# Optimization experiments

Hardware: AMD Instinct MI355X
Metric: run time of the kernel (lower is better)

## Reference

```python
import jax, jax.numpy as jnp
import numpy as np
import math

D_MODEL = 1024
D_ATTN = 128
D_MID = 128
L = 4096

def setup_inputs() -> dict:
    key = jax.random.key(0)
    ks = jax.random.split(key, 5)
    scale = 1.0 / math.sqrt(D_MODEL)
    return {
        "x": jax.random.normal(ks[0], (L, D_MODEL), jnp.float32),
        "z": jax.random.normal(ks[1], (L, D_MODEL), jnp.float32),
        "Wq": jax.random.normal(ks[2], (D_MODEL, D_ATTN), jnp.float32) * scale,
        "bq": jnp.zeros((D_ATTN,), jnp.float32),
        "Wk": jax.random.normal(ks[3], (D_MODEL, D_ATTN), jnp.float32) * scale,
        "bk": jnp.zeros((D_ATTN,), jnp.float32),
        "Wv": jax.random.normal(ks[4], (D_MODEL, D_MID), jnp.float32) * scale,
        "bv": jnp.zeros((D_MID,), jnp.float32),
    }

def reference(x, z, Wq, bq, Wk, bk, Wv, bv):
    # q: [L_x, d_attn], k: [L_z, d_attn], v: [L_z, d_mid]
    q = x @ Wq + bq
    k = z @ Wk + bk
    v = z @ Wv + bv
    inv_sqrt_d = 1.0 / math.sqrt(D_ATTN)
    s = (q @ k.T) * inv_sqrt_d            # [L_x, L_z]
    y = jax.nn.softmax(s, axis=-1) @ v    # [L_x, d_mid]
    return y
```

## Files before the change

kernel.cpp:

```cpp
#include <hip/hip_runtime.h>
#include <hip/hip_bf16.h>

typedef __attribute__((ext_vector_type(8))) short short8;
typedef __attribute__((ext_vector_type(4))) float f32x4;
typedef __attribute__((ext_vector_type(8))) _Float16 half8;

#define L_SEQ 4096
#define DM    1024
#define DA    128
#define AZ    16

#define OFF_QB  786432
#define OFF_KF  1835008
#define OFF_VF  2883584
#define OFF_OA  4063232
#define OA_BYTES ((size_t)AZ * L_SEQ * DA * 2)

__device__ __forceinline__ short f2bf(float f) {
    union { float f; unsigned u; } v; v.f = f;
    unsigned u = v.u;
    u += 0x7FFFu + ((u >> 16) & 1u);
    return (short)(u >> 16);
}

__device__ __forceinline__ unsigned cvt_pk_bf16(float lo, float hi) {
    unsigned r;
    asm("v_cvt_pk_bf16_f32 %0, %1, %2" : "=v"(r) : "v"(lo), "v"(hi));
    return r;
}

typedef const __attribute__((address_space(1))) void g_void_t;
typedef __attribute__((address_space(3))) void l_void_t;
__device__ __forceinline__ void g2lds16(const void* g, void* l) {
    __builtin_amdgcn_global_load_lds((g_void_t*)g, (l_void_t*)l, 16, 0, 0);
}

__global__ __launch_bounds__(256) void prep_w_kernel(
    const float* __restrict__ Wq, const float* __restrict__ Wk,
    const float* __restrict__ Wv, short8* __restrict__ WTf)
{
    const int m = blockIdx.y, kidx = blockIdx.x;
    const float* __restrict__ W = (m == 0) ? Wq : (m == 1) ? Wk : Wv;
    __shared__ __align__(16) float Ws[32 * 132];
    const int t = threadIdx.x;
#pragma unroll
    for (int i = 0; i < 4; i++) {
        const int u = i * 256 + t;
        const int kk = u >> 5, n4 = (u & 31) * 4;
        *(f32x4*)&Ws[kk * 132 + n4] = *(const f32x4*)&W[(size_t)(kidx * 32 + kk) * DA + n4];
    }
    __syncthreads();
#pragma unroll
    for (int i = 0; i < 2; i++) {
        const int u = i * 256 + t;
        const int nt = u >> 6, lane = u & 63, l16 = lane & 15, quad = lane >> 4;
        short8 fr;
#pragma unroll
        for (int j = 0; j < 8; j++)
            fr[j] = f2bf(Ws[(quad * 8 + j) * 132 + nt * 16 + l16]);
        WTf[((size_t)(m * 32 + kidx) * 8 + nt) * 64 + lane] = fr;
    }
}

__global__ __launch_bounds__(256, 1) void qkv_kernel(
    const float* __restrict__ x, const float* __restrict__ z,
    const char* __restrict__ WTraw,
    const float* __restrict__ bq, const float* __restrict__ bk,
    const float* __restrict__ bv,
    short* __restrict__ qb, short8* __restrict__ kf, short8* __restrict__ vf)
{
    __shared__ __align__(16) char smem[2][32768];

    const int t = threadIdx.x;
    const int wave = t >> 6, lane = t & 63;
    const int l16 = lane & 15, quad = lane >> 4;
    const int mtile = wave >> 1, nhalf = wave & 1;
    const int isKV = blockIdx.y;
    const int m1 = isKV ? 1 : 0;
    const int row0 = blockIdx.x * 32;
    const int nbytes = isKV ? 32768 : 16384;

    const float* __restrict__ Am = isKV ? z : x;
    const float* ap = Am + (size_t)(row0 + mtile * 16 + l16) * DM + quad * 8;

    f32x4 acc1[4], acc2[4];
#pragma unroll
    for (int i = 0; i < 4; i++) {
        acc1[i] = (f32x4){0.f, 0.f, 0.f, 0.f};
        acc2[i] = (f32x4){0.f, 0.f, 0.f, 0.f};
    }

    auto stage = [&](int it2, int b) {
        const char* base1 = WTraw + (size_t)(m1 * 32 + it2 * 2) * 8192;
        const char* base2 = WTraw + (size_t)(2 * 32 + it2 * 2) * 8192;
#pragma unroll
        for (int i = 0; i < 8; i++) {
            const int off = i * 4096 + wave * 1024;
            if (off < nbytes) {
                const char* src = (off < 16384) ? (base1 + off) : (base2 + (off - 16384));
                g2lds16(src + lane * 16, &smem[b][off]);
            }
        }
    };

    f32x4 cur[4], nxt[4];
#pragma unroll
    for (int j = 0; j < 2; j++) {
        cur[j * 2]     = *(const f32x4*)(ap + j * 32);
        cur[j * 2 + 1] = *(const f32x4*)(ap + j * 32 + 4);
        nxt[j * 2]     = *(const f32x4*)(ap + 64 + j * 32);
        nxt[j * 2 + 1] = *(const f32x4*)(ap + 64 + j * 32 + 4);
    }

    stage(0, 0);
    __syncthreads();

#pragma unroll 1
    for (int it = 0; it < 16; it++) {
        const int b = it & 1;
        if (it + 1 < 16) stage(it + 1, b ^ 1);

        const int ipf = (it + 2 < 16) ? it + 2 : it;
        f32x4 fut[4];
#pragma unroll
        for (int j = 0; j < 2; j++) {
            fut[j * 2]     = *(const f32x4*)(ap + ipf * 64 + j * 32);
            fut[j * 2 + 1] = *(const f32x4*)(ap + ipf * 64 + j * 32 + 4);
        }

#pragma unroll
        for (int ss = 0; ss < 2; ss++) {
            short8 afr;
#pragma unroll
            for (int j = 0; j < 4; j++) {
                afr[j]     = f2bf(cur[ss * 2][j]);
                afr[4 + j] = f2bf(cur[ss * 2 + 1][j]);
            }
#pragma unroll
            for (int ntl = 0; ntl < 4; ntl++) {
                short8 bfr = *(const short8*)&smem[b][ss * 8192 + ((nhalf * 4 + ntl) * 64 + lane) * 16];
                acc1[ntl] = __builtin_amdgcn_mfma_f32_16x16x32_bf16(afr, bfr, acc1[ntl], 0, 0, 0);
            }
            if (isKV) {
#pragma unroll
                for (int ntl = 0; ntl < 4; ntl++) {
                    short8 bfr = *(const short8*)&smem[b][16384 + ss * 8192 + ((nhalf * 4 + ntl) * 64 + lane) * 16];
                    acc2[ntl] = __builtin_amdgcn_mfma_f32_16x16x32_bf16(afr, bfr, acc2[ntl], 0, 0, 0);
                }
            }
        }
        __syncthreads();
#pragma unroll
        for (int j = 0; j < 4; j++) { cur[j] = nxt[j]; nxt[j] = fut[j]; }
    }

    if (!isKV) {
        const float CL2E = 0.1275187669712930f;
#pragma unroll
        for (int ntl = 0; ntl < 4; ntl++) {
            const int col = nhalf * 64 + ntl * 16 + l16;
            const float bb = bq[col];
#pragma unroll
            for (int r = 0; r < 4; r++)
                qb[(size_t)(row0 + mtile * 16 + quad * 4 + r) * DA + col] =
                    f2bf((acc1[ntl][r] + bb) * CL2E);
        }
        return;
    }

    short* kT = (short*)&smem[0][0];
    short* vT = (short*)&smem[0][16384];
#pragma unroll
    for (int ntl = 0; ntl < 4; ntl++) {
        const int col = nhalf * 64 + ntl * 16 + l16;
        const float bbk = bk[col], bbv = bv[col];
#pragma unroll
        for (int r = 0; r < 4; r++) {
            const int rl = mtile * 16 + quad * 4 + r;
            kT[rl * 132 + col] = f2bf(acc1[ntl][r] + bbk);
            vT[rl * 132 + col] = f2bf(acc2[ntl][r] + bbv);
        }
    }
    __syncthreads();

    const int kg = blockIdx.x;
#pragma unroll
    for (int i = 0; i < 2; i++) {
        const int f = i * 256 + t;
        const int ks = f >> 7, nth = (f >> 6) & 1, ln = f & 63;
        const int lf = ln & 15, qf = ln >> 4;
        short8 fr;
#pragma unroll
        for (int j = 0; j < 8; j++)
            fr[j] = kT[(nth * 16 + lf) * 132 + ks * 32 + qf * 8 + j];
        kf[((size_t)(kg * 4 + ks) * 2 + nth) * 64 + ln] = fr;
    }
#pragma unroll
    for (int i = 0; i < 2; i++) {
        const int f = i * 256 + t;
        const int nt = f >> 6, ln = f & 63;
        const int lf = ln & 15, qf = ln >> 4;
        short8 fr;
#pragma unroll
        for (int j = 0; j < 8; j++)
            fr[j] = vT[(qf * 8 + j) * 132 + nt * 16 + lf];
        vf[((size_t)kg * 8 + nt) * 64 + ln] = fr;
    }
}

__global__ __launch_bounds__(256, 2) void attn_kernel(
    const short* __restrict__ qb, const char* __restrict__ kfg,
    const char* __restrict__ vfg, _Float16* __restrict__ OA,
    float* __restrict__ lA)
{
    __shared__ __align__(16) char kv[2][16384];
    __shared__ __align__(16) short Ps[4][2][32 * 40];

    const int t    = threadIdx.x;
    const int wave = t >> 6;
    const int lane = t & 63;
    const int l16  = lane & 15;
    const int quad = lane >> 4;
    const int qr0  = blockIdx.x * 128;
    const int g0   = blockIdx.y * 8;

    auto stage = [&](int g, int b) {
        const char* kb_ = kfg + (size_t)(g0 + g) * 8192;
        const char* vb_ = vfg + (size_t)(g0 + g) * 8192;
#pragma unroll
        for (int i = 0; i < 4; i++) {
            const int off = i * 4096 + wave * 1024;
            const char* src = (off < 8192) ? (kb_ + off) : (vb_ + (off - 8192));
            g2lds16(src + lane * 16, &kv[b][off]);
        }
    };

    stage(0, 0);

    short8 af[2][4];
#pragma unroll
    for (int mt = 0; mt < 2; mt++) {
        const short* qrow = qb + (size_t)(qr0 + wave * 32 + mt * 16 + l16) * DA + quad * 8;
#pragma unroll
        for (int ks = 0; ks < 4; ks++)
            af[mt][ks] = *(const short8*)(qrow + ks * 32);
    }

    short8 bones;
#pragma unroll
    for (int j = 0; j < 8; j++) bones[j] = (l16 == 0) ? (short)0x3F80 : (short)0;

    f32x4 O[2][9];
#pragma unroll
    for (int mt = 0; mt < 2; mt++)
#pragma unroll
        for (int i = 0; i < 9; i++) O[mt][i] = (f32x4){0.f, 0.f, 0.f, 0.f};

    short8 bvC[8];

    __syncthreads();

#pragma unroll 1
    for (int g = 0; g < 8; g++) {
        const int b = g & 1;
        if (g + 1 < 8) stage(g + 1, b ^ 1);

        const char* kb_ = &kv[b][0];
        const char* vb_ = &kv[b][8192];

        f32x4 s0[2][2];
#pragma unroll
        for (int mt = 0; mt < 2; mt++)
#pragma unroll
            for (int nh = 0; nh < 2; nh++) s0[mt][nh] = (f32x4){0.f, 0.f, 0.f, 0.f};
#pragma unroll
        for (int ks = 0; ks < 4; ks++)
#pragma unroll
            for (int nh = 0; nh < 2; nh++) {
                const short8 bfr = *(const short8*)(kb_ + ((ks * 2 + nh) * 64 + lane) * 16);
                s0[0][nh] = __builtin_amdgcn_mfma_f32_16x16x32_bf16(af[0][ks], bfr, s0[0][nh], 0, 0, 0);
                s0[1][nh] = __builtin_amdgcn_mfma_f32_16x16x32_bf16(af[1][ks], bfr, s0[1][nh], 0, 0, 0);
            }

        short8 bvN[8];
#pragma unroll
        for (int nt = 0; nt < 8; nt++)
            bvN[nt] = *(const short8*)(vb_ + (nt * 64 + lane) * 16);

        short8 a2[2];
        if (g > 0) {
            const short* Pp = &Ps[wave][b ^ 1][0];
            a2[0] = *(const short8*)&Pp[l16 * 40 + quad * 8];
            a2[1] = *(const short8*)&Pp[(16 + l16) * 40 + quad * 8];
        }

        short* P = &Ps[wave][b][0];
#pragma unroll
        for (int mt = 0; mt < 2; mt++)
#pragma unroll
            for (int nh = 0; nh < 2; nh++)
#pragma unroll
                for (int rp = 0; rp < 2; rp++) {
                    const float e0 = exp2f(s0[mt][nh][rp * 2]);
                    const float e1 = exp2f(s0[mt][nh][rp * 2 + 1]);
                    const unsigned pk = cvt_pk_bf16(e0, e1);
                    const int row = mt * 16 + quad * 4 + rp * 2;
                    P[row * 40 + nh * 16 + l16]       = (short)(pk & 0xffff);
                    P[(row + 1) * 40 + nh * 16 + l16] = (short)(pk >> 16);
                }

        if (g > 0) {
#pragma unroll
            for (int nt = 0; nt < 8; nt++) {
                O[0][nt] = __builtin_amdgcn_mfma_f32_16x16x32_bf16(a2[0], bvC[nt], O[0][nt], 0, 0, 0);
                O[1][nt] = __builtin_amdgcn_mfma_f32_16x16x32_bf16(a2[1], bvC[nt], O[1][nt], 0, 0, 0);
            }
            O[0][8] = __builtin_amdgcn_mfma_f32_16x16x32_bf16(a2[0], bones, O[0][8], 0, 0, 0);
            O[1][8] = __builtin_amdgcn_mfma_f32_16x16x32_bf16(a2[1], bones, O[1][8], 0, 0, 0);
        }

#pragma unroll
        for (int nt = 0; nt < 8; nt++) bvC[nt] = bvN[nt];

        __syncthreads();
    }

    {
        const short* Pp = &Ps[wave][1][0];
        short8 a2[2];
        a2[0] = *(const short8*)&Pp[l16 * 40 + quad * 8];
        a2[1] = *(const short8*)&Pp[(16 + l16) * 40 + quad * 8];
#pragma unroll
        for (int nt = 0; nt < 8; nt++) {
            O[0][nt] = __builtin_amdgcn_mfma_f32_16x16x32_bf16(a2[0], bvC[nt], O[0][nt], 0, 0, 0);
            O[1][nt] = __builtin_amdgcn_mfma_f32_16x16x32_bf16(a2[1], bvC[nt], O[1][nt], 0, 0, 0);
        }
        O[0][8] = __builtin_amdgcn_mfma_f32_16x16x32_bf16(a2[0], bones, O[0][8], 0, 0, 0);
        O[1][8] = __builtin_amdgcn_mfma_f32_16x16x32_bf16(a2[1], bones, O[1][8], 0, 0, 0);
    }

    const int rw = qr0 + wave * 32;
    _Float16* Ob = OA + (size_t)blockIdx.y * L_SEQ * DA;
#pragma unroll
    for (int mt = 0; mt < 2; mt++)
#pragma unroll
        for (int nt = 0; nt < 8; nt++)
#pragma unroll
            for (int r = 0; r < 4; r++)
                Ob[(size_t)(rw + mt * 16 + quad * 4 + r) * DA + nt * 16 + l16] =
                    (_Float16)O[mt][nt][r];
    if (l16 == 0) {
        float* lb = lA + (size_t)blockIdx.y * L_SEQ;
#pragma unroll
        for (int mt = 0; mt < 2; mt++)
#pragma unroll
            for (int r = 0; r < 4; r++)
                lb[rw + mt * 16 + quad * 4 + r] = O[mt][8][r];
    }
}

__global__ __launch_bounds__(256) void merge_kernel(
    const _Float16* __restrict__ OA, const float* __restrict__ lA,
    float* __restrict__ out)
{
    const int t = threadIdx.x;
    const int row = blockIdx.x * 16 + (t >> 4);
    const int cg = (t & 15) * 8;

    float acc[8];
#pragma unroll
    for (int j = 0; j < 8; j++) acc[j] = 0.f;
    float lsum = 0.f;
#pragma unroll
    for (int zz = 0; zz < AZ; zz++) {
        const half8 v = *(const half8*)&OA[((size_t)zz * L_SEQ + row) * DA + cg];
#pragma unroll
        for (int j = 0; j < 8; j++) acc[j] += (float)v[j];
        lsum += lA[(size_t)zz * L_SEQ + row];
    }
    const float inv = 1.f / lsum;
    f32x4 o0, o1;
#pragma unroll
    for (int j = 0; j < 4; j++) { o0[j] = acc[j] * inv; o1[j] = acc[4 + j] * inv; }
    f32x4* dst = (f32x4*)&out[(size_t)row * DA + cg];
    dst[0] = o0;
    dst[1] = o1;
}

extern "C" void kernel_launch(void* const* d_in, const int* in_sizes, int n_in,
                              void* d_out, int out_size, void* d_ws, size_t ws_size,
                              hipStream_t stream) {
    (void)in_sizes; (void)n_in; (void)out_size; (void)ws_size;
    const float* x  = (const float*)d_in[0];
    const float* z  = (const float*)d_in[1];
    const float* Wq = (const float*)d_in[2];
    const float* bq = (const float*)d_in[3];
    const float* Wk = (const float*)d_in[4];
    const float* bk = (const float*)d_in[5];
    const float* Wv = (const float*)d_in[6];
    const float* bv = (const float*)d_in[7];
    float* out = (float*)d_out;

    short8*   WTf = (short8*)d_ws;
    short*    qb  = (short*)((char*)d_ws + OFF_QB);
    short8*   kf  = (short8*)((char*)d_ws + OFF_KF);
    short8*   vf  = (short8*)((char*)d_ws + OFF_VF);
    _Float16* OA  = (_Float16*)((char*)d_ws + OFF_OA);
    float*    lA  = (float*)((char*)d_ws + OFF_OA + OA_BYTES);

    prep_w_kernel<<<dim3(32, 3), 256, 0, stream>>>(Wq, Wk, Wv, WTf);
    qkv_kernel<<<dim3(128, 2), 256, 0, stream>>>(x, z, (const char*)WTf,
                                                 bq, bk, bv, qb, kf, vf);
    attn_kernel<<<dim3(32, AZ), 256, 0, stream>>>(qb, (const char*)kf,
                                                  (const char*)vf, OA, lA);
    merge_kernel<<<256, 256, 0, stream>>>(OA, lA, out);
}
```

Before: 127.9 us.

## Keep softmax probabilities in registers via transposed QK and cross-lane permutes

Computes S transposed (K fragment as the A operand) so each lane holds exp values along the key dimension. It then uses v_permlane32_swap and ds_swizzle to rearrange the packed bf16 pairs directly into the A-operand layout for the PV MFMA. This removes the per-wave LDS staging buffer for P and the one-iteration software pipeline of PV behind QK. The cost is extra permute and select instructions, and the loss of the overlap that deferring PV used to provide.

```diff
diff --git a/kernel.cpp b/kernel.cpp
--- a/kernel.cpp
+++ b/kernel.cpp
@@ -214,7 +214,6 @@
     float* __restrict__ lA)
 {
     __shared__ __align__(16) char kv[2][16384];
-    __shared__ __align__(16) short Ps[4][2][32 * 40];
 
     const int t    = threadIdx.x;
     const int wave = t >> 6;
@@ -256,8 +255,6 @@
 #pragma unroll
         for (int i = 0; i < 9; i++) O[mt][i] = (f32x4){0.f, 0.f, 0.f, 0.f};
 
-    short8 bvC[8];
-
     __syncthreads();
 
 #pragma unroll 1
@@ -268,75 +265,55 @@
         const char* kb_ = &kv[b][0];
         const char* vb_ = &kv[b][8192];
 
-        f32x4 s0[2][2];
-#pragma unroll
-        for (int mt = 0; mt < 2; mt++)
-#pragma unroll
-            for (int nh = 0; nh < 2; nh++) s0[mt][nh] = (f32x4){0.f, 0.f, 0.f, 0.f};
+        f32x4 st[2][2];
+#pragma unroll
+        for (int zh = 0; zh < 2; zh++)
+#pragma unroll
+            for (int mt = 0; mt < 2; mt++) st[zh][mt] = (f32x4){0.f, 0.f, 0.f, 0.f};
 #pragma unroll
         for (int ks = 0; ks < 4; ks++)
 #pragma unroll
-            for (int nh = 0; nh < 2; nh++) {
-                const short8 bfr = *(const short8*)(kb_ + ((ks * 2 + nh) * 64 + lane) * 16);
-                s0[0][nh] = __builtin_amdgcn_mfma_f32_16x16x32_bf16(af[0][ks], bfr, s0[0][nh], 0, 0, 0);
-                s0[1][nh] = __builtin_amdgcn_mfma_f32_16x16x32_bf16(af[1][ks], bfr, s0[1][nh], 0, 0, 0);
-            }
-
-        short8 bvN[8];
+            for (int zh = 0; zh < 2; zh++) {
+                const short8 kfr = *(const short8*)(kb_ + ((ks * 2 + zh) * 64 + lane) * 16);
+                st[zh][0] = __builtin_amdgcn_mfma_f32_16x16x32_bf16(kfr, af[0][ks], st[zh][0], 0, 0, 0);
+                st[zh][1] = __builtin_amdgcn_mfma_f32_16x16x32_bf16(kfr, af[1][ks], st[zh][1], 0, 0, 0);
+            }
+
+        short8 b2v[8];
 #pragma unroll
         for (int nt = 0; nt < 8; nt++)
-            bvN[nt] = *(const short8*)(vb_ + (nt * 64 + lane) * 16);
+            b2v[nt] = *(const short8*)(vb_ + (nt * 64 + lane) * 16);
 
         short8 a2[2];
-        if (g > 0) {
-            const short* Pp = &Ps[wave][b ^ 1][0];
-            a2[0] = *(const short8*)&Pp[l16 * 40 + quad * 8];
-            a2[1] = *(const short8*)&Pp[(16 + l16) * 40 + quad * 8];
-        }
-
-        short* P = &Ps[wave][b][0];
-#pragma unroll
-        for (int mt = 0; mt < 2; mt++)
-#pragma unroll
-            for (int nh = 0; nh < 2; nh++)
-#pragma unroll
-                for (int rp = 0; rp < 2; rp++) {
-                    const float e0 = exp2f(s0[mt][nh][rp * 2]);
-                    const float e1 = exp2f(s0[mt][nh][rp * 2 + 1]);
-                    const unsigned pk = cvt_pk_bf16(e0, e1);
-                    const int row = mt * 16 + quad * 4 + rp * 2;
-                    P[row * 40 + nh * 16 + l16]       = (short)(pk & 0xffff);
-                    P[(row + 1) * 40 + nh * 16 + l16] = (short)(pk >> 16);
-                }
-
-        if (g > 0) {
-#pragma unroll
-            for (int nt = 0; nt < 8; nt++) {
-                O[0][nt] = __builtin_amdgcn_mfma_f32_16x16x32_bf16(a2[0], bvC[nt], O[0][nt], 0, 0, 0);
-                O[1][nt] = __builtin_amdgcn_mfma_f32_16x16x32_bf16(a2[1], bvC[nt], O[1][nt], 0, 0, 0);
-            }
-            O[0][8] = __builtin_amdgcn_mfma_f32_16x16x32_bf16(a2[0], bones, O[0][8], 0, 0, 0);
-            O[1][8] = __builtin_amdgcn_mfma_f32_16x16x32_bf16(a2[1], bones, O[1][8], 0, 0, 0);
-        }
-
-#pragma unroll
-        for (int nt = 0; nt < 8; nt++) bvC[nt] = bvN[nt];
-
-        __syncthreads();
-    }
-
-    {
-        const short* Pp = &Ps[wave][1][0];
-        short8 a2[2];
-        a2[0] = *(const short8*)&Pp[l16 * 40 + quad * 8];
-        a2[1] = *(const short8*)&Pp[(16 + l16) * 40 + quad * 8];
+#pragma unroll
+        for (int mt = 0; mt < 2; mt++) {
+            unsigned x0 = cvt_pk_bf16(exp2f(st[0][mt][0]), exp2f(st[0][mt][1]));
+            unsigned x1 = cvt_pk_bf16(exp2f(st[0][mt][2]), exp2f(st[0][mt][3]));
+            unsigned y0 = cvt_pk_bf16(exp2f(st[1][mt][0]), exp2f(st[1][mt][1]));
+            unsigned y1 = cvt_pk_bf16(exp2f(st[1][mt][2]), exp2f(st[1][mt][3]));
+            asm volatile("v_permlane32_swap_b32 %0, %1" : "+v"(x0), "+v"(y0));
+            asm volatile("v_permlane32_swap_b32 %0, %1" : "+v"(x1), "+v"(y1));
+            const unsigned Asw0 = __builtin_amdgcn_ds_swizzle((int)x0, 0x401F);
+            const unsigned Asw1 = __builtin_amdgcn_ds_swizzle((int)x1, 0x401F);
+            const unsigned Bsw0 = __builtin_amdgcn_ds_swizzle((int)y0, 0x401F);
+            const unsigned Bsw1 = __builtin_amdgcn_ds_swizzle((int)y1, 0x401F);
+            const bool hiq = (quad & 1) != 0;
+            union { short8 s; unsigned u[4]; } pa;
+            pa.u[0] = hiq ? Bsw0 : x0;
+            pa.u[1] = hiq ? Bsw1 : x1;
+            pa.u[2] = hiq ? y0   : Asw0;
+            pa.u[3] = hiq ? y1   : Asw1;
+            a2[mt] = pa.s;
+        }
+
 #pragma unroll
         for (int nt = 0; nt < 8; nt++) {
-            O[0][nt] = __builtin_amdgcn_mfma_f32_16x16x32_bf16(a2[0], bvC[nt], O[0][nt], 0, 0, 0);
-            O[1][nt] = __builtin_amdgcn_mfma_f32_16x16x32_bf16(a2[1], bvC[nt], O[1][nt], 0, 0, 0);
+            O[0][nt] = __builtin_amdgcn_mfma_f32_16x16x32_bf16(a2[0], b2v[nt], O[0][nt], 0, 0, 0);
+            O[1][nt] = __builtin_amdgcn_mfma_f32_16x16x32_bf16(a2[1], b2v[nt], O[1][nt], 0, 0, 0);
         }
         O[0][8] = __builtin_amdgcn_mfma_f32_16x16x32_bf16(a2[0], bones, O[0][8], 0, 0, 0);
         O[1][8] = __builtin_amdgcn_mfma_f32_16x16x32_bf16(a2[1], bones, O[1][8], 0, 0, 0);
+        __syncthreads();
     }
 
     const int rw = qr0 + wave * 32;
```

Result: no change. 126.7 us (-0.9%).
